# Kernel optimization log

Measured on AMD Instinct MI355X. Metric: run time of the kernel, lower is better.

The kernel has to match this reference:

```python
import jax, jax.numpy as jnp
import numpy as np

B, T, D, H = 2, 2048, 1024, 16  # batch, seq_len, d_model (d_in==d_out), num_heads
HD = D // H  # head_dim = 64


def setup_inputs() -> dict:
    key = jax.random.key(0)
    ks = jax.random.split(key, 6)
    s = 1.0 / np.sqrt(D)
    return {
        "x": jax.random.normal(ks[0], (B, T, D), dtype=jnp.float32),
        "wq": jax.random.normal(ks[1], (D, D), dtype=jnp.float32) * s,
        "wk": jax.random.normal(ks[2], (D, D), dtype=jnp.float32) * s,
        "wv": jax.random.normal(ks[3], (D, D), dtype=jnp.float32) * s,
        "wo": jax.random.normal(ks[4], (D, D), dtype=jnp.float32) * s,
        "bo": jax.random.normal(ks[5], (D,), dtype=jnp.float32) * 0.01,
    }


def reference(x, wq, wk, wv, wo, bo):
    b, t, d = x.shape
    # projections (qkv_bias=False), split heads: [b, h, t, hd]
    q = (x @ wq).reshape(b, t, H, HD).transpose(0, 2, 1, 3)
    k = (x @ wk).reshape(b, t, H, HD).transpose(0, 2, 1, 3)
    v = (x @ wv).reshape(b, t, H, HD).transpose(0, 2, 1, 3)
    # causal attention scores [b, h, t, t]
    scores = jnp.einsum("bhqd,bhkd->bhqk", q, k) / jnp.sqrt(jnp.float32(HD))
    causal = jnp.tril(jnp.ones((t, t), dtype=bool))
    scores = jnp.where(causal[None, None, :, :], scores, -jnp.inf)
    attn = jax.nn.softmax(scores, axis=-1)  # dropout p=0.0 -> identity
    ctx = jnp.einsum("bhqk,bhkd->bhqd", attn, v)  # [b, h, t, hd]
    ctx = ctx.transpose(0, 2, 1, 3).reshape(b, t, d)  # merge heads
    return ctx @ wo + bo
```

## Files before the change

### kernel.cpp

```cpp
#include <hip/hip_runtime.h>
#include <hip/hip_bf16.h>
#include <stdint.h>

#define B_  2
#define T_  2048
#define D_  1024
#define H_  16
#define HD_ 64

typedef __bf16 bf16x8 __attribute__((ext_vector_type(8)));
typedef __bf16 bf16x4 __attribute__((ext_vector_type(4)));
typedef float  f32x4  __attribute__((ext_vector_type(4)));

__device__ __forceinline__ void async_copy16(const void* g, void* l) {
  __builtin_amdgcn_global_load_lds((__attribute__((address_space(1))) void*)(g),
                                   (__attribute__((address_space(3))) void*)(l),
                                   16, 0, 0);
}

__global__ void prep_kernel(const float* __restrict__ x,
                            const float* __restrict__ wq, const float* __restrict__ wk,
                            const float* __restrict__ wv, const float* __restrict__ wo,
                            __bf16* __restrict__ xc,
                            __bf16* __restrict__ wqkv_t, __bf16* __restrict__ wo_t) {
  const int id  = blockIdx.x;
  const int tid = threadIdx.x;
  if (id < 4096) {
    __shared__ __bf16 tile[32][33];
    const int z   = id >> 10;
    const int rem = id & 1023;
    const int n0 = (rem & 31) * 32, k0 = (rem >> 5) * 32;
    const int tx = tid & 31, ty = tid >> 5;
    const float* src = (z == 0) ? wq : (z == 1) ? wk : (z == 2) ? wv : wo;
    __bf16* dst = (z < 3) ? (wqkv_t + (size_t)z * 1024 * 1024) : wo_t;
#pragma unroll
    for (int i = 0; i < 4; ++i)
      tile[ty + 8 * i][tx] = (__bf16)src[(size_t)(k0 + ty + 8 * i) * 1024 + n0 + tx];
    __syncthreads();
#pragma unroll
    for (int i = 0; i < 4; ++i)
      dst[(size_t)(n0 + ty + 8 * i) * 1024 + k0 + tx] = tile[tx][ty + 8 * i];
  } else {
    const int i0 = ((id - 4096) * 256 + tid) * 4;
    const f32x4 f = *(const f32x4*)(x + i0);
    bf16x4 v;
#pragma unroll
    for (int k = 0; k < 4; ++k) v[k] = (__bf16)f[k];
    *(bf16x4*)(xc + i0) = v;
  }
}

template <int MODE>
__launch_bounds__(256)
__global__ void gemm128_kernel(const __bf16* __restrict__ A, const __bf16* __restrict__ Bt, int K,
                               __bf16* __restrict__ q_b, __bf16* __restrict__ k_b,
                               __bf16* __restrict__ vt_b,
                               const float* __restrict__ bo, float* __restrict__ outp) {
  __shared__ __align__(16) __bf16 As[128 * 64];
  __shared__ __align__(16) __bf16 Bs[128 * 64];
  const int tid  = threadIdx.x;
  const int w    = tid >> 6, lane = tid & 63;
  const int quad = lane >> 4, lr = lane & 15;

  const int orig = blockIdx.x;
  int bx, by;
  if (MODE == 0) {
    const int wgid = (orig & 7) * 96 + (orig >> 3);
    bx = wgid >> 5;
    by = wgid & 31;
  } else {
    const int wgid = (orig & 7) * 32 + (orig >> 3);
    bx = wgid & 7;
    by = wgid >> 3;
  }
  const int tm = by * 128, tn = bx * 128;
  const int wm = (w >> 1) * 64, wn = (w & 1) * 64;
  const int lrow   = lane >> 3;
  const int gchunk = (lane & 7) ^ lrow;

  f32x4 acc[4][4] = {};

  for (int k0 = 0; k0 < K; k0 += 64) {
#pragma unroll
    for (int c = 0; c < 4; ++c) {
      const int chunk = w * 4 + c;
      const int row   = chunk * 8 + lrow;
      async_copy16(A  + (size_t)(tm + row) * K + k0 + gchunk * 8, As + chunk * 512);
      async_copy16(Bt + (size_t)(tn + row) * K + k0 + gchunk * 8, Bs + chunk * 512);
    }
    __syncthreads();
#pragma unroll
    for (int ks = 0; ks < 2; ++ks) {
      bf16x8 af[4], bfr[4];
#pragma unroll
      for (int mi = 0; mi < 4; ++mi) {
        const int row = wm + mi * 16 + lr;
        const int ch  = (ks * 4 + quad) ^ (row & 7);
        af[mi] = *(const bf16x8*)(As + row * 64 + ch * 8);
      }
#pragma unroll
      for (int ni = 0; ni < 4; ++ni) {
        const int row = wn + ni * 16 + lr;
        const int ch  = (ks * 4 + quad) ^ (row & 7);
        bfr[ni] = *(const bf16x8*)(Bs + row * 64 + ch * 8);
      }
#pragma unroll
      for (int mi = 0; mi < 4; ++mi)
#pragma unroll
        for (int ni = 0; ni < 4; ++ni)
          acc[mi][ni] = __builtin_amdgcn_mfma_f32_16x16x32_bf16(af[mi], bfr[ni], acc[mi][ni], 0, 0, 0);
    }
    __syncthreads();
  }

  if (MODE == 0) {
#pragma unroll
    for (int mi = 0; mi < 4; ++mi) {
      const int mrow0 = tm + wm + mi * 16 + quad * 4;
      const int b  = mrow0 >> 11;
      const int t0 = mrow0 & 2047;
#pragma unroll
      for (int ni = 0; ni < 4; ++ni) {
        const int ncol = tn + wn + ni * 16 + lr;
        const int mat  = ncol >> 10;
        const int nn   = ncol & 1023;
        const int h = nn >> 6, hd = nn & 63;
        if (mat == 0) {
#pragma unroll
          for (int r = 0; r < 4; ++r)
            q_b[((size_t)((b * H_ + h) * T_ + t0 + r)) * HD_ + hd] =
                (__bf16)(acc[mi][ni][r] * 0.125f);
        } else if (mat == 1) {
#pragma unroll
          for (int r = 0; r < 4; ++r)
            k_b[((size_t)((b * H_ + h) * T_ + t0 + r)) * HD_ + hd] =
                (__bf16)(acc[mi][ni][r]);
        } else {
          bf16x4 pk;
#pragma unroll
          for (int r = 0; r < 4; ++r) pk[r] = (__bf16)(acc[mi][ni][r]);
          *(bf16x4*)(vt_b + ((size_t)(b * H_ + h) * HD_ + hd) * T_ + t0) = pk;
        }
      }
    }
  } else {
#pragma unroll
    for (int mi = 0; mi < 4; ++mi) {
      const int m0 = tm + wm + mi * 16 + quad * 4;
#pragma unroll
      for (int ni = 0; ni < 4; ++ni) {
        const int n = tn + wn + ni * 16 + lr;
        const float bias = bo[n];
#pragma unroll
        for (int r = 0; r < 4; ++r)
          outp[(size_t)(m0 + r) * D_ + n] = acc[mi][ni][r] + bias;
      }
    }
  }
}

__launch_bounds__(256, 3)
__global__ void attn_kernel(const __bf16* __restrict__ q_b, const __bf16* __restrict__ k_b,
                            const __bf16* __restrict__ vt_b, __bf16* __restrict__ ctx) {
  __shared__ __align__(16) __bf16 sK[64 * 64];
  __shared__ __align__(16) __bf16 sV[64 * 64];
  __shared__ __align__(16) __bf16 sP[2][64][72];
  const int tid  = threadIdx.x;
  const int w    = tid >> 6, lane = tid & 63;
  const int quad = lane >> 4, lr = lane & 15;
  const int id = blockIdx.x;
  const int bh  = (id & 7) * 4 + ((id >> 3) & 3);
  const int t0i = (id >> 5) & 7;
  const int rnd = id >> 8;
  const int tq  = (3 - rnd) * 8 + ((rnd & 1) ? t0i : (7 - t0i));
  const __bf16* qh = q_b  + (size_t)bh * T_ * HD_;
  const __bf16* kh = k_b  + (size_t)bh * T_ * HD_;
  const __bf16* vh = vt_b + (size_t)bh * HD_ * T_;
  const int b = bh >> 4, h = bh & 15;

  const int r0 = tid >> 3, r1 = (tid + 256) >> 3;
  const int g0 = tid & 7;

  const int q0 = tq * 64;
  const int nj = tq + 1;
  const int w16 = w * 16;

  bf16x8 qf[4][2];
#pragma unroll
  for (int qs = 0; qs < 4; ++qs)
#pragma unroll
    for (int ks = 0; ks < 2; ++ks)
      qf[qs][ks] = *(const bf16x8*)(qh + (size_t)(q0 + qs * 16 + lr) * HD_ + ks * 32 + quad * 8);

  bf16x8 onesf;
#pragma unroll
  for (int j = 0; j < 8; ++j) onesf[j] = (__bf16)1.0f;

  f32x4 o[4] = {};
  f32x4 ls = {};

  bf16x8 kr0 = *(const bf16x8*)(kh + (size_t)r0 * HD_ + g0 * 8);
  bf16x8 kr1 = *(const bf16x8*)(kh + (size_t)r1 * HD_ + g0 * 8);
  bf16x8 vr0 = *(const bf16x8*)(vh + (size_t)r0 * T_ + g0 * 8);
  bf16x8 vr1 = *(const bf16x8*)(vh + (size_t)r1 * T_ + g0 * 8);

  for (int j = 0; j < nj; ++j) {
    const int j0 = j * 64;
    const int pb = j & 1;
    __syncthreads();
    *(bf16x8*)(sK + r0 * 64 + (g0 ^ (r0 & 7)) * 8) = kr0;
    *(bf16x8*)(sK + r1 * 64 + (g0 ^ (r1 & 7)) * 8) = kr1;
    *(bf16x8*)(sV + r0 * 64 + (g0 ^ (r0 & 7)) * 8) = vr0;
    *(bf16x8*)(sV + r1 * 64 + (g0 ^ (r1 & 7)) * 8) = vr1;
    __syncthreads();
    if (j + 1 < nj) {
      const int jn = j0 + 64;
      kr0 = *(const bf16x8*)(kh + (size_t)(jn + r0) * HD_ + g0 * 8);
      kr1 = *(const bf16x8*)(kh + (size_t)(jn + r1) * HD_ + g0 * 8);
      vr0 = *(const bf16x8*)(vh + (size_t)r0 * T_ + jn + g0 * 8);
      vr1 = *(const bf16x8*)(vh + (size_t)r1 * T_ + jn + g0 * 8);
    }
    const int krow = w16 + lr;
    bf16x8 kf[2];
    kf[0] = *(const bf16x8*)(sK + krow * 64 + ((quad) ^ (krow & 7)) * 8);
    kf[1] = *(const bf16x8*)(sK + krow * 64 + ((4 + quad) ^ (krow & 7)) * 8);
    f32x4 s[4] = {};
    __builtin_amdgcn_s_setprio(1);
#pragma unroll
    for (int qs = 0; qs < 4; ++qs) {
      s[qs] = __builtin_amdgcn_mfma_f32_16x16x32_bf16(qf[qs][0], kf[0], s[qs], 0, 0, 0);
      s[qs] = __builtin_amdgcn_mfma_f32_16x16x32_bf16(qf[qs][1], kf[1], s[qs], 0, 0, 0);
    }
    __builtin_amdgcn_s_setprio(0);
    if (j0 + 63 > q0) {
      const int col = j0 + w16 + lr;
#pragma unroll
      for (int qs = 0; qs < 4; ++qs)
#pragma unroll
        for (int r = 0; r < 4; ++r) {
          const int row = q0 + qs * 16 + quad * 4 + r;
          if (col > row) s[qs][r] = -3.0e38f;
        }
    }
#pragma unroll
    for (int qs = 0; qs < 4; ++qs)
#pragma unroll
      for (int r = 0; r < 4; ++r)
        s[qs][r] = __expf(s[qs][r]);
#pragma unroll
    for (int qs = 0; qs < 4; ++qs)
#pragma unroll
      for (int r = 0; r < 4; ++r)
        sP[pb][qs * 16 + quad * 4 + r][w16 + lr] = (__bf16)s[qs][r];
    __syncthreads();
    bf16x8 pf[2];
#pragma unroll
    for (int ks = 0; ks < 2; ++ks)
      pf[ks] = *(const bf16x8*)(&sP[pb][w16 + lr][ks * 32 + quad * 8]);
    __builtin_amdgcn_s_setprio(1);
#pragma unroll
    for (int ni = 0; ni < 4; ++ni) {
      const int row = ni * 16 + lr;
#pragma unroll
      for (int ks = 0; ks < 2; ++ks) {
        const int ch = (ks * 4 + quad) ^ (row & 7);
        bf16x8 vf = *(const bf16x8*)(sV + row * 64 + ch * 8);
        o[ni] = __builtin_amdgcn_mfma_f32_16x16x32_bf16(pf[ks], vf, o[ni], 0, 0, 0);
      }
    }
    ls = __builtin_amdgcn_mfma_f32_16x16x32_bf16(pf[0], onesf, ls, 0, 0, 0);
    ls = __builtin_amdgcn_mfma_f32_16x16x32_bf16(pf[1], onesf, ls, 0, 0, 0);
    __builtin_amdgcn_s_setprio(0);
  }
#pragma unroll
  for (int r = 0; r < 4; ++r) {
    const float inv = 1.0f / ls[r];
    const int t = q0 + w16 + quad * 4 + r;
#pragma unroll
    for (int ni = 0; ni < 4; ++ni)
      ctx[((size_t)(b * T_ + t)) * D_ + h * HD_ + ni * 16 + lr] =
          (__bf16)(o[ni][r] * inv);
  }
}

extern "C" void kernel_launch(void* const* d_in, const int* in_sizes, int n_in,
                              void* d_out, int out_size, void* d_ws, size_t ws_size,
                              hipStream_t stream) {
  (void)in_sizes; (void)n_in; (void)out_size; (void)ws_size;
  const float* x  = (const float*)d_in[0];
  const float* wq = (const float*)d_in[1];
  const float* wk = (const float*)d_in[2];
  const float* wv = (const float*)d_in[3];
  const float* wo = (const float*)d_in[4];
  const float* bo = (const float*)d_in[5];
  float* outp = (float*)d_out;

  char* ws = (char*)d_ws;
  __bf16* ctx    = (__bf16*)(ws + 0);
  __bf16* wqkv_t = (__bf16*)(ws + 0);
  __bf16* wo_t   = (__bf16*)(ws + 8388608);
  __bf16* q_b    = (__bf16*)(ws + 10485760);
  __bf16* k_b    = (__bf16*)(ws + 18874368);
  __bf16* vt_b   = (__bf16*)(ws + 27262976);
  __bf16* xc     = (__bf16*)(ws + 35651584);

  prep_kernel<<<8192, 256, 0, stream>>>(x, wq, wk, wv, wo, xc, wqkv_t, wo_t);
  gemm128_kernel<0><<<768, 256, 0, stream>>>(xc, wqkv_t, 1024, q_b, k_b, vt_b, nullptr, nullptr);
  attn_kernel<<<1024, 256, 0, stream>>>(q_b, k_b, vt_b, ctx);
  gemm128_kernel<1><<<256, 256, 0, stream>>>(ctx, wo_t, 1024, nullptr, nullptr, nullptr, bo, outp);
}
```

Measured before the change: 172.6 us.

## Load K fragments straight from global and compute transposed scores for vectorized P stores

Removes the shared-memory K tile: each lane loads its K MFMA fragment directly from global memory and prefetches the next tile's fragment into registers. The QK^T MFMA is issued with operands swapped, so each lane holds four consecutive key columns for one query row. That lets the bf16 probabilities go to shared memory as one 8-byte vector store instead of four scalar stores. This cuts LDS traffic and shared-memory footprint, at the cost of more uncoalesced-per-lane global loads and a few extra registers.

```diff
diff --git a/kernel.cpp b/kernel.cpp
--- a/kernel.cpp
+++ b/kernel.cpp
@@ -162,7 +162,6 @@
 __launch_bounds__(256, 3)
 __global__ void attn_kernel(const __bf16* __restrict__ q_b, const __bf16* __restrict__ k_b,
                             const __bf16* __restrict__ vt_b, __bf16* __restrict__ ctx) {
-  __shared__ __align__(16) __bf16 sK[64 * 64];
   __shared__ __align__(16) __bf16 sV[64 * 64];
   __shared__ __align__(16) __bf16 sP[2][64][72];
   const int tid  = threadIdx.x;
@@ -199,8 +198,11 @@
   f32x4 o[4] = {};
   f32x4 ls = {};
 
-  bf16x8 kr0 = *(const bf16x8*)(kh + (size_t)r0 * HD_ + g0 * 8);
-  bf16x8 kr1 = *(const bf16x8*)(kh + (size_t)r1 * HD_ + g0 * 8);
+  const __bf16* kr = kh + (size_t)(w16 + lr) * HD_;
+  bf16x8 kf0 = *(const bf16x8*)(kr + quad * 8);
+  bf16x8 kf1 = *(const bf16x8*)(kr + 32 + quad * 8);
+  bf16x8 kn0, kn1;
+
   bf16x8 vr0 = *(const bf16x8*)(vh + (size_t)r0 * T_ + g0 * 8);
   bf16x8 vr1 = *(const bf16x8*)(vh + (size_t)r1 * T_ + g0 * 8);
 
@@ -208,50 +210,47 @@
     const int j0 = j * 64;
     const int pb = j & 1;
     __syncthreads();
-    *(bf16x8*)(sK + r0 * 64 + (g0 ^ (r0 & 7)) * 8) = kr0;
-    *(bf16x8*)(sK + r1 * 64 + (g0 ^ (r1 & 7)) * 8) = kr1;
     *(bf16x8*)(sV + r0 * 64 + (g0 ^ (r0 & 7)) * 8) = vr0;
     *(bf16x8*)(sV + r1 * 64 + (g0 ^ (r1 & 7)) * 8) = vr1;
     __syncthreads();
     if (j + 1 < nj) {
       const int jn = j0 + 64;
-      kr0 = *(const bf16x8*)(kh + (size_t)(jn + r0) * HD_ + g0 * 8);
-      kr1 = *(const bf16x8*)(kh + (size_t)(jn + r1) * HD_ + g0 * 8);
       vr0 = *(const bf16x8*)(vh + (size_t)r0 * T_ + jn + g0 * 8);
       vr1 = *(const bf16x8*)(vh + (size_t)r1 * T_ + jn + g0 * 8);
-    }
-    const int krow = w16 + lr;
-    bf16x8 kf[2];
-    kf[0] = *(const bf16x8*)(sK + krow * 64 + ((quad) ^ (krow & 7)) * 8);
-    kf[1] = *(const bf16x8*)(sK + krow * 64 + ((4 + quad) ^ (krow & 7)) * 8);
-    f32x4 s[4] = {};
+      kn0 = *(const bf16x8*)(kr + (size_t)jn * HD_ + quad * 8);
+      kn1 = *(const bf16x8*)(kr + (size_t)jn * HD_ + 32 + quad * 8);
+    }
+    f32x4 ns[4] = {};
     __builtin_amdgcn_s_setprio(1);
 #pragma unroll
-    for (int qs = 0; qs < 4; ++qs) {
-      s[qs] = __builtin_amdgcn_mfma_f32_16x16x32_bf16(qf[qs][0], kf[0], s[qs], 0, 0, 0);
-      s[qs] = __builtin_amdgcn_mfma_f32_16x16x32_bf16(qf[qs][1], kf[1], s[qs], 0, 0, 0);
+    for (int qb = 0; qb < 4; ++qb) {
+      ns[qb] = __builtin_amdgcn_mfma_f32_16x16x32_bf16(kf0, qf[qb][0], ns[qb], 0, 0, 0);
+      ns[qb] = __builtin_amdgcn_mfma_f32_16x16x32_bf16(kf1, qf[qb][1], ns[qb], 0, 0, 0);
     }
     __builtin_amdgcn_s_setprio(0);
+    if (j + 1 < nj) { kf0 = kn0; kf1 = kn1; }
     if (j0 + 63 > q0) {
-      const int col = j0 + w16 + lr;
-#pragma unroll
-      for (int qs = 0; qs < 4; ++qs)
-#pragma unroll
-        for (int r = 0; r < 4; ++r) {
-          const int row = q0 + qs * 16 + quad * 4 + r;
-          if (col > row) s[qs][r] = -3.0e38f;
-        }
-    }
-#pragma unroll
-    for (int qs = 0; qs < 4; ++qs)
+      const int kvb = j0 + w16 + quad * 4;
+#pragma unroll
+      for (int qb = 0; qb < 4; ++qb) {
+        const int qg = q0 + qb * 16 + lr;
+#pragma unroll
+        for (int r = 0; r < 4; ++r)
+          if (kvb + r > qg) ns[qb][r] = -3.0e38f;
+      }
+    }
+#pragma unroll
+    for (int qb = 0; qb < 4; ++qb)
 #pragma unroll
       for (int r = 0; r < 4; ++r)
-        s[qs][r] = __expf(s[qs][r]);
-#pragma unroll
-    for (int qs = 0; qs < 4; ++qs)
-#pragma unroll
-      for (int r = 0; r < 4; ++r)
-        sP[pb][qs * 16 + quad * 4 + r][w16 + lr] = (__bf16)s[qs][r];
+        ns[qb][r] = __expf(ns[qb][r]);
+#pragma unroll
+    for (int qb = 0; qb < 4; ++qb) {
+      bf16x4 pk;
+#pragma unroll
+      for (int r = 0; r < 4; ++r) pk[r] = (__bf16)ns[qb][r];
+      *(bf16x4*)(&sP[pb][qb * 16 + lr][w16 + quad * 4]) = pk;
+    }
     __syncthreads();
     bf16x8 pf[2];
 #pragma unroll
```

New measurement: 172.3 us. About the same (-0.2%).
